# Optimization experiments

Measured on AMD Instinct MI355X. Metric: run time of the kernel, lower is better.

Reference implementation:

```python
import jax, jax.numpy as jnp
import numpy as np

N = 100000
E = 1600000
F_IN = 4
HID = 8
HEADS = 8
NEG_SLOPE = 0.2


def setup_inputs() -> dict:
    key = jax.random.key(0)
    ks = jax.random.split(key, 12)
    x = jax.random.normal(ks[0], (N, F_IN), dtype=jnp.float32)
    edge_index = jax.random.randint(ks[1], (2, E), 0, N, dtype=jnp.int64)
    s = 0.3
    W1 = jax.random.normal(ks[2], (F_IN, HEADS * HID), dtype=jnp.float32) * s
    att_src1 = jax.random.normal(ks[3], (HEADS, HID), dtype=jnp.float32) * s
    att_dst1 = jax.random.normal(ks[4], (HEADS, HID), dtype=jnp.float32) * s
    b1 = jnp.zeros((HEADS * HID,), dtype=jnp.float32)
    W2 = jax.random.normal(ks[5], (HEADS * HID, 1), dtype=jnp.float32) * s
    att_src2 = jax.random.normal(ks[6], (1, 1), dtype=jnp.float32) * s
    att_dst2 = jax.random.normal(ks[7], (1, 1), dtype=jnp.float32) * s
    b2 = jnp.zeros((1,), dtype=jnp.float32)
    return {"x": x, "edge_index": edge_index, "W1": W1, "att_src1": att_src1,
            "att_dst1": att_dst1, "b1": b1, "W2": W2, "att_src2": att_src2,
            "att_dst2": att_dst2, "b2": b2}


def gat_conv(x, src, dst, W, att_s, att_d, b, heads, out_ch, concat):
    n = x.shape[0]
    h = (x @ W).reshape(n, heads, out_ch)              # [N,H,C]
    a_s = jnp.sum(h * att_s, axis=-1)                  # [N,H]
    a_d = jnp.sum(h * att_d, axis=-1)                  # [N,H]
    e = jax.nn.leaky_relu(a_s[src] + a_d[dst], NEG_SLOPE)  # [E,H]
    # segment softmax over edges grouped by destination node
    m = jax.ops.segment_max(e, dst, num_segments=n)
    e = jnp.exp(e - m[dst])
    denom = jax.ops.segment_sum(e, dst, num_segments=n)
    alpha = e / (denom[dst] + 1e-16)                   # [E,H]
    msg = h[src] * alpha[..., None]                    # [E,H,C]
    out = jax.ops.segment_sum(msg, dst, num_segments=n)  # [N,H,C]
    out = out.reshape(n, heads * out_ch) if concat else out.mean(axis=1)
    return out + b


def reference(x, edge_index, W1, att_src1, att_dst1, b1, W2, att_src2, att_dst2, b2):
    n = x.shape[0]
    loops = jnp.arange(n, dtype=edge_index.dtype)
    src = jnp.concatenate([edge_index[0], loops])
    dst = jnp.concatenate([edge_index[1], loops])
    h = gat_conv(x, src, dst, W1, att_src1, att_dst1, b1, HEADS, HID, True)
    h = jax.nn.elu(h)
    out = gat_conv(h, src, dst, W2, att_src2, att_dst2, b2, 1, 1, False)
    return jax.nn.sigmoid(out)
```

## Files before the change

### kernel.cpp

```cpp
#include <hip/hip_runtime.h>

#define NN 100000
#define NE 1600000
#define NBKT 391
#define CAP 8192
#define TILE 4096
#define NTILE ((NE + TILE - 1) / TILE)
#define NEG 0.2f

__global__ __launch_bounds__(512) void kU_prep(
    const float* __restrict__ W1, const float* __restrict__ atts,
    const float* __restrict__ attd, float* __restrict__ us, float* __restrict__ ud,
    int* __restrict__ bcnt, int* __restrict__ row)
{
    int t = threadIdx.x;
    if (t < NBKT) bcnt[t] = 0;
    if (t == 0) row[NN] = NE;
    if (t < 64) {
        int half = t >> 5;
        int i = t & 31;
        int h = i >> 2, k = i & 3;
        const float* att = half ? attd : atts;
        float acc = 0.f;
        #pragma unroll
        for (int j = 0; j < 8; j++)
            acc += W1[k * 64 + h * 8 + j] * att[h * 8 + j];
        (half ? ud : us)[h * 4 + k] = acc;
    }
}

__global__ __launch_bounds__(1024) void kP1_tile(
    const int* __restrict__ ei, int* __restrict__ bcnt, unsigned* __restrict__ bpack)
{
    __shared__ unsigned sarr[TILE];
    __shared__ int lh[512], lsc[512], lgb[512];
    int t = threadIdx.x;
    int e0 = blockIdx.x * TILE;
    int n = NE - e0; if (n > TILE) n = TILE;

    if (t < 512) lh[t] = 0;
    __syncthreads();
    for (int i = t; i < n; i += 1024) {
        int d = ei[NE + e0 + i];
        atomicAdd(&lh[d >> 8], 1);
    }
    __syncthreads();
    if (t < 512) lsc[t] = lh[t];
    __syncthreads();
    #pragma unroll
    for (int o = 1; o < 512; o <<= 1) {
        int u = 0;
        if (t < 512 && t >= o) u = lsc[t - o];
        __syncthreads();
        if (t < 512) lsc[t] += u;
        __syncthreads();
    }
    if (t < NBKT && lh[t] > 0) lgb[t] = atomicAdd(&bcnt[t], lh[t]);
    __syncthreads();
    if (t < 512) lh[t] = lsc[t] - lh[t];
    __syncthreads();
    for (int i = t; i < n; i += 1024) {
        int s = ei[e0 + i], d = ei[NE + e0 + i];
        int b = d >> 8;
        int pos = atomicAdd(&lh[b], 1);
        sarr[pos] = ((unsigned)s << 8) | (unsigned)(d & 255);
    }
    __syncthreads();
    int wave = t >> 6, lane = t & 63;
    for (int b = wave; b < NBKT; b += 16) {
        int start = (b == 0) ? 0 : lsc[b - 1];
        int cntb = lsc[b] - start;
        if (cntb == 0) continue;
        int gb = lgb[b];
        unsigned* dstp = &bpack[(size_t)b * CAP];
        for (int j = lane; j < cntb; j += 64) {
            int gpos = gb + j;
            if (gpos < CAP) dstp[gpos] = sarr[start + j];
        }
    }
}

__global__ __launch_bounds__(1024) void kP2_build(
    const int* __restrict__ bcnt, const unsigned* __restrict__ bpack,
    int* __restrict__ row, int* __restrict__ esrc)
{
    __shared__ int lh[256], lsc[256], lcur[256];
    __shared__ int sbs[512];
    __shared__ int sarr[CAP];
    int b = blockIdx.x;
    int t = threadIdx.x;
    if (t < 512) sbs[t] = (t < b) ? bcnt[t] : 0;
    __syncthreads();
    #pragma unroll
    for (int o = 256; o > 0; o >>= 1) {
        if (t < o) sbs[t] += sbs[t + o];
        __syncthreads();
    }
    int base = sbs[0];
    int cnt = bcnt[b];
    if (cnt > CAP) cnt = CAP;
    const unsigned* bp = &bpack[(size_t)b * CAP];
    if (t < 256) lh[t] = 0;
    __syncthreads();
    for (int i = t; i < cnt; i += 1024)
        atomicAdd(&lh[bp[i] & 255u], 1);
    __syncthreads();
    if (t < 256) lsc[t] = lh[t];
    __syncthreads();
    #pragma unroll
    for (int o = 1; o < 256; o <<= 1) {
        int u = 0;
        if (t < 256 && t >= o) u = lsc[t - o];
        __syncthreads();
        if (t < 256) lsc[t] += u;
        __syncthreads();
    }
    if (t < 256) {
        int ex = lsc[t] - lh[t];
        lcur[t] = ex;
        int node = b * 256 + t;
        if (node < NN) row[node] = base + ex;
    }
    __syncthreads();
    for (int i = t; i < cnt; i += 1024) {
        unsigned u = bp[i];
        int pos = atomicAdd(&lcur[u & 255u], 1);
        sarr[pos] = (int)(u >> 8);
    }
    __syncthreads();
    for (int i = t; i < cnt; i += 1024)
        esrc[base + i] = sarr[i];
}

__global__ __launch_bounds__(256) void kE_l1agg(
    const int* __restrict__ row, const int* __restrict__ esrc,
    const float* __restrict__ x, const float* __restrict__ us,
    const float* __restrict__ ud, const float* __restrict__ W1,
    const float* __restrict__ b1, const float* __restrict__ W2,
    float* __restrict__ h2)
{
    int t = threadIdx.x;
    int grp = t >> 3;
    int h   = t & 7;
    int dst = blockIdx.x * 32 + grp;
    if (dst >= NN) return;

    int start = row[dst], end = row[dst + 1];
    int m = end - start;

    float4 u  = *reinterpret_cast<const float4*>(&us[h * 4]);
    float4 vd = *reinterpret_cast<const float4*>(&ud[h * 4]);
    float4 xd = *reinterpret_cast<const float4*>(&x[(size_t)dst * 4]);
    float adj = xd.x * vd.x + xd.y * vd.y + xd.z * vd.z + xd.w * vd.w;

    float a0 = fmaf(xd.x, u.x, fmaf(xd.y, u.y, fmaf(xd.z, u.z, fmaf(xd.w, u.w, adj))));
    a0 = fmaxf(a0, NEG * a0);
    float p0 = __expf(a0);
    float den = p0;
    float xa0 = p0 * xd.x, xa1 = p0 * xd.y, xa2 = p0 * xd.z, xa3 = p0 * xd.w;

    int j = 0;
    for (; j + 4 <= m; j += 4) {
        int s0 = esrc[start + j];
        int s1 = esrc[start + j + 1];
        int s2 = esrc[start + j + 2];
        int s3 = esrc[start + j + 3];
        float4 q0 = *reinterpret_cast<const float4*>(&x[(size_t)s0 * 4]);
        float4 q1 = *reinterpret_cast<const float4*>(&x[(size_t)s1 * 4]);
        float4 q2 = *reinterpret_cast<const float4*>(&x[(size_t)s2 * 4]);
        float4 q3 = *reinterpret_cast<const float4*>(&x[(size_t)s3 * 4]);
        float b0 = fmaf(q0.x, u.x, fmaf(q0.y, u.y, fmaf(q0.z, u.z, fmaf(q0.w, u.w, adj))));
        float b1v = fmaf(q1.x, u.x, fmaf(q1.y, u.y, fmaf(q1.z, u.z, fmaf(q1.w, u.w, adj))));
        float b2v = fmaf(q2.x, u.x, fmaf(q2.y, u.y, fmaf(q2.z, u.z, fmaf(q2.w, u.w, adj))));
        float b3v = fmaf(q3.x, u.x, fmaf(q3.y, u.y, fmaf(q3.z, u.z, fmaf(q3.w, u.w, adj))));
        b0  = fmaxf(b0,  NEG * b0);
        b1v = fmaxf(b1v, NEG * b1v);
        b2v = fmaxf(b2v, NEG * b2v);
        b3v = fmaxf(b3v, NEG * b3v);
        float pa = __expf(b0);
        float pb = __expf(b1v);
        float pc = __expf(b2v);
        float pd = __expf(b3v);
        den += (pa + pb) + (pc + pd);
        xa0 = fmaf(pa, q0.x, fmaf(pb, q1.x, fmaf(pc, q2.x, fmaf(pd, q3.x, xa0))));
        xa1 = fmaf(pa, q0.y, fmaf(pb, q1.y, fmaf(pc, q2.y, fmaf(pd, q3.y, xa1))));
        xa2 = fmaf(pa, q0.z, fmaf(pb, q1.z, fmaf(pc, q2.z, fmaf(pd, q3.z, xa2))));
        xa3 = fmaf(pa, q0.w, fmaf(pb, q1.w, fmaf(pc, q2.w, fmaf(pd, q3.w, xa3))));
    }
    for (; j < m; ++j) {
        int s0 = esrc[start + j];
        float4 q0 = *reinterpret_cast<const float4*>(&x[(size_t)s0 * 4]);
        float b0 = fmaf(q0.x, u.x, fmaf(q0.y, u.y, fmaf(q0.z, u.z, fmaf(q0.w, u.w, adj))));
        b0 = fmaxf(b0, NEG * b0);
        float pb = __expf(b0);
        den += pb;
        xa0 = fmaf(pb, q0.x, xa0);
        xa1 = fmaf(pb, q0.y, xa1);
        xa2 = fmaf(pb, q0.z, xa2);
        xa3 = fmaf(pb, q0.w, xa3);
    }

    int c0 = h * 8;
    float4 w0l = *reinterpret_cast<const float4*>(&W1[c0]);
    float4 w0h = *reinterpret_cast<const float4*>(&W1[c0 + 4]);
    float4 w1l = *reinterpret_cast<const float4*>(&W1[64 + c0]);
    float4 w1h = *reinterpret_cast<const float4*>(&W1[64 + c0 + 4]);
    float4 w2l = *reinterpret_cast<const float4*>(&W1[128 + c0]);
    float4 w2h = *reinterpret_cast<const float4*>(&W1[128 + c0 + 4]);
    float4 w3l = *reinterpret_cast<const float4*>(&W1[192 + c0]);
    float4 w3h = *reinterpret_cast<const float4*>(&W1[192 + c0 + 4]);
    float4 bbl = *reinterpret_cast<const float4*>(&b1[c0]);
    float4 bbh = *reinterpret_cast<const float4*>(&b1[c0 + 4]);
    float4 wwl = *reinterpret_cast<const float4*>(&W2[c0]);
    float4 wwh = *reinterpret_cast<const float4*>(&W2[c0 + 4]);
    float inv = 1.f / (den + 1e-16f);

    float acc = 0.f;
    {
        float v;
        v = (xa0*w0l.x + xa1*w1l.x + xa2*w2l.x + xa3*w3l.x)*inv + bbl.x;
        v = v > 0.f ? v : (__expf(v) - 1.f);  acc += v * wwl.x;
        v = (xa0*w0l.y + xa1*w1l.y + xa2*w2l.y + xa3*w3l.y)*inv + bbl.y;
        v = v > 0.f ? v : (__expf(v) - 1.f);  acc += v * wwl.y;
        v = (xa0*w0l.z + xa1*w1l.z + xa2*w2l.z + xa3*w3l.z)*inv + bbl.z;
        v = v > 0.f ? v : (__expf(v) - 1.f);  acc += v * wwl.z;
        v = (xa0*w0l.w + xa1*w1l.w + xa2*w2l.w + xa3*w3l.w)*inv + bbl.w;
        v = v > 0.f ? v : (__expf(v) - 1.f);  acc += v * wwl.w;
        v = (xa0*w0h.x + xa1*w1h.x + xa2*w2h.x + xa3*w3h.x)*inv + bbh.x;
        v = v > 0.f ? v : (__expf(v) - 1.f);  acc += v * wwh.x;
        v = (xa0*w0h.y + xa1*w1h.y + xa2*w2h.y + xa3*w3h.y)*inv + bbh.y;
        v = v > 0.f ? v : (__expf(v) - 1.f);  acc += v * wwh.y;
        v = (xa0*w0h.z + xa1*w1h.z + xa2*w2h.z + xa3*w3h.z)*inv + bbh.z;
        v = v > 0.f ? v : (__expf(v) - 1.f);  acc += v * wwh.z;
        v = (xa0*w0h.w + xa1*w1h.w + xa2*w2h.w + xa3*w3h.w)*inv + bbh.w;
        v = v > 0.f ? v : (__expf(v) - 1.f);  acc += v * wwh.w;
    }
    acc += __shfl_xor(acc, 1, 8);
    acc += __shfl_xor(acc, 2, 8);
    acc += __shfl_xor(acc, 4, 8);
    if (h == 0) h2[dst] = acc;
}

__global__ __launch_bounds__(256) void kF_l2agg(
    const int* __restrict__ row, const int* __restrict__ esrc,
    const float* __restrict__ h2, const float* __restrict__ as2,
    const float* __restrict__ ad2, const float* __restrict__ b2,
    float* __restrict__ out)
{
    int t = threadIdx.x;
    int grp = t >> 3;
    int sub = t & 7;
    int dst = blockIdx.x * 32 + grp;
    if (dst >= NN) return;
    int start = row[dst], end = row[dst + 1];
    float a_s = as2[0], a_d = ad2[0];
    float hdv = h2[dst];
    float hd = hdv * a_d;

    float den = 0.f, num = 0.f;
    if (sub == 0) {
        float v = hdv * a_s + hd;
        v = fmaxf(v, NEG * v);
        float p = __expf(v);
        den = p;
        num = p * hdv;
    }
    int i = start + sub;
    for (; i + 24 < end; i += 32) {
        float hs0 = h2[esrc[i]];
        float hs1 = h2[esrc[i + 8]];
        float hs2 = h2[esrc[i + 16]];
        float hs3 = h2[esrc[i + 24]];
        float v0 = fmaf(hs0, a_s, hd);
        float v1 = fmaf(hs1, a_s, hd);
        float v2 = fmaf(hs2, a_s, hd);
        float v3 = fmaf(hs3, a_s, hd);
        v0 = fmaxf(v0, NEG * v0);
        v1 = fmaxf(v1, NEG * v1);
        v2 = fmaxf(v2, NEG * v2);
        v3 = fmaxf(v3, NEG * v3);
        float p0 = __expf(v0);
        float p1 = __expf(v1);
        float p2 = __expf(v2);
        float p3 = __expf(v3);
        den += (p0 + p1) + (p2 + p3);
        num = fmaf(p0, hs0, fmaf(p1, hs1, fmaf(p2, hs2, fmaf(p3, hs3, num))));
    }
    for (; i < end; i += 8) {
        float hs = h2[esrc[i]];
        float v = fmaf(hs, a_s, hd);
        v = fmaxf(v, NEG * v);
        float p = __expf(v);
        den += p;
        num = fmaf(p, hs, num);
    }
    den += __shfl_xor(den, 1, 8);
    num += __shfl_xor(num, 1, 8);
    den += __shfl_xor(den, 2, 8);
    num += __shfl_xor(num, 2, 8);
    den += __shfl_xor(den, 4, 8);
    num += __shfl_xor(num, 4, 8);
    if (sub == 0) {
        float v = num / (den + 1e-16f) + b2[0];
        out[dst] = 1.f / (1.f + __expf(-v));
    }
}

extern "C" void kernel_launch(void* const* d_in, const int* in_sizes, int n_in,
                              void* d_out, int out_size, void* d_ws, size_t ws_size,
                              hipStream_t stream) {
    const float* x     = (const float*)d_in[0];
    const int*   ei    = (const int*)d_in[1];
    const float* W1    = (const float*)d_in[2];
    const float* atts1 = (const float*)d_in[3];
    const float* attd1 = (const float*)d_in[4];
    const float* b1    = (const float*)d_in[5];
    const float* W2    = (const float*)d_in[6];
    const float* atts2 = (const float*)d_in[7];
    const float* attd2 = (const float*)d_in[8];
    const float* b2    = (const float*)d_in[9];
    float* out = (float*)d_out;

    float* w = (float*)d_ws;
    float* us = w;
    float* ud = w + 32;
    float* h2 = w + 64;
    int* ibase  = (int*)(w + 64 + (size_t)NN);
    int* bcnt   = ibase;
    int* row    = ibase + 512;
    int* esrc   = ibase + 512 + NN + 64;
    unsigned* bpack = (unsigned*)(ibase + 512 + NN + 64 + NE);

    dim3 gG((NN + 31) / 32);

    hipLaunchKernelGGL(kU_prep, dim3(1), dim3(512), 0, stream, W1, atts1, attd1, us, ud, bcnt, row);
    hipLaunchKernelGGL(kP1_tile, dim3(NTILE), dim3(1024), 0, stream, ei, bcnt, bpack);
    hipLaunchKernelGGL(kP2_build, dim3(NBKT), dim3(1024), 0, stream, bcnt, bpack, row, esrc);
    hipLaunchKernelGGL(kE_l1agg, gG, dim3(256), 0, stream, row, esrc, x, us, ud, W1, b1, W2, h2);
    hipLaunchKernelGGL(kF_l2agg, gG, dim3(256), 0, stream, row, esrc, h2, atts2, attd2, b2, out);
}
```

Before: 71.66 us.

## Use fixed-capacity bucket CSR with (start,count) rows and drop prep kernel

Switches the CSR layout so each 256-node bucket gets a fixed CAP-sized slot in esrc, with each node storing (start, degree) as int2. This removes the cross-bucket prefix reduction and the shared staging buffer in the build kernel, which now scatters directly to global memory. The attention-projection prep is folded into the layer-1 kernel via shared memory, the counter reset becomes a memset, and the partition kernels drop from 1024 to 512 threads. The costs are that every layer-1 block recomputes the small projection, esrc writes become uncoalesced scatters, and edge lists become sparse in memory.

```diff
diff --git a/kernel.cpp b/kernel.cpp
--- a/kernel.cpp
+++ b/kernel.cpp
@@ -8,28 +8,7 @@
 #define NTILE ((NE + TILE - 1) / TILE)
 #define NEG 0.2f
 
-__global__ __launch_bounds__(512) void kU_prep(
-    const float* __restrict__ W1, const float* __restrict__ atts,
-    const float* __restrict__ attd, float* __restrict__ us, float* __restrict__ ud,
-    int* __restrict__ bcnt, int* __restrict__ row)
-{
-    int t = threadIdx.x;
-    if (t < NBKT) bcnt[t] = 0;
-    if (t == 0) row[NN] = NE;
-    if (t < 64) {
-        int half = t >> 5;
-        int i = t & 31;
-        int h = i >> 2, k = i & 3;
-        const float* att = half ? attd : atts;
-        float acc = 0.f;
-        #pragma unroll
-        for (int j = 0; j < 8; j++)
-            acc += W1[k * 64 + h * 8 + j] * att[h * 8 + j];
-        (half ? ud : us)[h * 4 + k] = acc;
-    }
-}
-
-__global__ __launch_bounds__(1024) void kP1_tile(
+__global__ __launch_bounds__(512) void kP1_tile(
     const int* __restrict__ ei, int* __restrict__ bcnt, unsigned* __restrict__ bpack)
 {
     __shared__ unsigned sarr[TILE];
@@ -38,28 +17,27 @@
     int e0 = blockIdx.x * TILE;
     int n = NE - e0; if (n > TILE) n = TILE;
 
-    if (t < 512) lh[t] = 0;
-    __syncthreads();
-    for (int i = t; i < n; i += 1024) {
+    lh[t] = 0;
+    __syncthreads();
+    for (int i = t; i < n; i += 512) {
         int d = ei[NE + e0 + i];
         atomicAdd(&lh[d >> 8], 1);
     }
     __syncthreads();
-    if (t < 512) lsc[t] = lh[t];
+    lsc[t] = lh[t];
     __syncthreads();
     #pragma unroll
     for (int o = 1; o < 512; o <<= 1) {
-        int u = 0;
-        if (t < 512 && t >= o) u = lsc[t - o];
+        int u = (t >= o) ? lsc[t - o] : 0;
         __syncthreads();
-        if (t < 512) lsc[t] += u;
+        lsc[t] += u;
         __syncthreads();
     }
     if (t < NBKT && lh[t] > 0) lgb[t] = atomicAdd(&bcnt[t], lh[t]);
     __syncthreads();
-    if (t < 512) lh[t] = lsc[t] - lh[t];
-    __syncthreads();
-    for (int i = t; i < n; i += 1024) {
+    lh[t] = lsc[t] - lh[t];
+    __syncthreads();
+    for (int i = t; i < n; i += 512) {
         int s = ei[e0 + i], d = ei[NE + e0 + i];
         int b = d >> 8;
         int pos = atomicAdd(&lh[b], 1);
@@ -67,7 +45,7 @@
     }
     __syncthreads();
     int wave = t >> 6, lane = t & 63;
-    for (int b = wave; b < NBKT; b += 16) {
+    for (int b = wave; b < NBKT; b += 8) {
         int start = (b == 0) ? 0 : lsc[b - 1];
         int cntb = lsc[b] - start;
         if (cntb == 0) continue;
@@ -80,29 +58,20 @@
     }
 }
 
-__global__ __launch_bounds__(1024) void kP2_build(
+__global__ __launch_bounds__(512) void kP2_build(
     const int* __restrict__ bcnt, const unsigned* __restrict__ bpack,
-    int* __restrict__ row, int* __restrict__ esrc)
+    int2* __restrict__ rowsd, int* __restrict__ esrc)
 {
     __shared__ int lh[256], lsc[256], lcur[256];
-    __shared__ int sbs[512];
-    __shared__ int sarr[CAP];
     int b = blockIdx.x;
     int t = threadIdx.x;
-    if (t < 512) sbs[t] = (t < b) ? bcnt[t] : 0;
-    __syncthreads();
-    #pragma unroll
-    for (int o = 256; o > 0; o >>= 1) {
-        if (t < o) sbs[t] += sbs[t + o];
-        __syncthreads();
-    }
-    int base = sbs[0];
     int cnt = bcnt[b];
     if (cnt > CAP) cnt = CAP;
     const unsigned* bp = &bpack[(size_t)b * CAP];
+    int base = b * CAP;
     if (t < 256) lh[t] = 0;
     __syncthreads();
-    for (int i = t; i < cnt; i += 1024)
+    for (int i = t; i < cnt; i += 512)
         atomicAdd(&lh[bp[i] & 255u], 1);
     __syncthreads();
     if (t < 256) lsc[t] = lh[t];
@@ -119,37 +88,47 @@
         int ex = lsc[t] - lh[t];
         lcur[t] = ex;
         int node = b * 256 + t;
-        if (node < NN) row[node] = base + ex;
-    }
-    __syncthreads();
-    for (int i = t; i < cnt; i += 1024) {
+        if (node < NN) rowsd[node] = make_int2(base + ex, lh[t]);
+    }
+    __syncthreads();
+    for (int i = t; i < cnt; i += 512) {
         unsigned u = bp[i];
         int pos = atomicAdd(&lcur[u & 255u], 1);
-        sarr[pos] = (int)(u >> 8);
-    }
-    __syncthreads();
-    for (int i = t; i < cnt; i += 1024)
-        esrc[base + i] = sarr[i];
+        esrc[base + pos] = (int)(u >> 8);
+    }
 }
 
 __global__ __launch_bounds__(256) void kE_l1agg(
-    const int* __restrict__ row, const int* __restrict__ esrc,
-    const float* __restrict__ x, const float* __restrict__ us,
-    const float* __restrict__ ud, const float* __restrict__ W1,
+    const int2* __restrict__ rowsd, const int* __restrict__ esrc,
+    const float* __restrict__ x, const float* __restrict__ atts,
+    const float* __restrict__ attd, const float* __restrict__ W1,
     const float* __restrict__ b1, const float* __restrict__ W2,
     float* __restrict__ h2)
 {
+    __shared__ float sus[32], sud[32];
     int t = threadIdx.x;
+    if (t < 64) {
+        int half = t >> 5;
+        int i = t & 31;
+        int hh = i >> 2, k = i & 3;
+        const float* att = half ? attd : atts;
+        float acc = 0.f;
+        #pragma unroll
+        for (int j = 0; j < 8; j++)
+            acc += W1[k * 64 + hh * 8 + j] * att[hh * 8 + j];
+        (half ? sud : sus)[hh * 4 + k] = acc;
+    }
+    __syncthreads();
+
     int grp = t >> 3;
     int h   = t & 7;
     int dst = blockIdx.x * 32 + grp;
-    if (dst >= NN) return;
-
-    int start = row[dst], end = row[dst + 1];
-    int m = end - start;
-
-    float4 u  = *reinterpret_cast<const float4*>(&us[h * 4]);
-    float4 vd = *reinterpret_cast<const float4*>(&ud[h * 4]);
+
+    int2 rd = rowsd[dst];
+    int start = rd.x, m = rd.y;
+
+    float4 u  = *reinterpret_cast<const float4*>(&sus[h * 4]);
+    float4 vd = *reinterpret_cast<const float4*>(&sud[h * 4]);
     float4 xd = *reinterpret_cast<const float4*>(&x[(size_t)dst * 4]);
     float adj = xd.x * vd.x + xd.y * vd.y + xd.z * vd.z + xd.w * vd.w;
 
@@ -242,7 +221,7 @@
 }
 
 __global__ __launch_bounds__(256) void kF_l2agg(
-    const int* __restrict__ row, const int* __restrict__ esrc,
+    const int2* __restrict__ rowsd, const int* __restrict__ esrc,
     const float* __restrict__ h2, const float* __restrict__ as2,
     const float* __restrict__ ad2, const float* __restrict__ b2,
     float* __restrict__ out)
@@ -251,8 +230,8 @@
     int grp = t >> 3;
     int sub = t & 7;
     int dst = blockIdx.x * 32 + grp;
-    if (dst >= NN) return;
-    int start = row[dst], end = row[dst + 1];
+    int2 rd = rowsd[dst];
+    int start = rd.x, end = rd.x + rd.y;
     float a_s = as2[0], a_d = ad2[0];
     float hdv = h2[dst];
     float hd = hdv * a_d;
@@ -322,20 +301,18 @@
     float* out = (float*)d_out;
 
     float* w = (float*)d_ws;
-    float* us = w;
-    float* ud = w + 32;
-    float* h2 = w + 64;
-    int* ibase  = (int*)(w + 64 + (size_t)NN);
-    int* bcnt   = ibase;
-    int* row    = ibase + 512;
-    int* esrc   = ibase + 512 + NN + 64;
-    unsigned* bpack = (unsigned*)(ibase + 512 + NN + 64 + NE);
-
-    dim3 gG((NN + 31) / 32);
-
-    hipLaunchKernelGGL(kU_prep, dim3(1), dim3(512), 0, stream, W1, atts1, attd1, us, ud, bcnt, row);
-    hipLaunchKernelGGL(kP1_tile, dim3(NTILE), dim3(1024), 0, stream, ei, bcnt, bpack);
-    hipLaunchKernelGGL(kP2_build, dim3(NBKT), dim3(1024), 0, stream, bcnt, bpack, row, esrc);
-    hipLaunchKernelGGL(kE_l1agg, gG, dim3(256), 0, stream, row, esrc, x, us, ud, W1, b1, W2, h2);
-    hipLaunchKernelGGL(kF_l2agg, gG, dim3(256), 0, stream, row, esrc, h2, atts2, attd2, b2, out);
-}
+    float* h2 = w;
+    int*  ibase = (int*)(w + (size_t)NN);
+    int2* rowsd = (int2*)ibase;
+    int*  bcnt  = ibase + (size_t)2 * NN;
+    int*  esrc  = ibase + (size_t)2 * NN + 512;
+    unsigned* bpack = (unsigned*)(esrc + (size_t)NBKT * CAP);
+
+    dim3 gG(NN / 32);
+
+    hipMemsetAsync(bcnt, 0, NBKT * sizeof(int), stream);
+    hipLaunchKernelGGL(kP1_tile, dim3(NTILE), dim3(512), 0, stream, ei, bcnt, bpack);
+    hipLaunchKernelGGL(kP2_build, dim3(NBKT), dim3(512), 0, stream, bcnt, bpack, rowsd, esrc);
+    hipLaunchKernelGGL(kE_l1agg, gG, dim3(256), 0, stream, rowsd, esrc, x, atts1, attd1, W1, b1, W2, h2);
+    hipLaunchKernelGGL(kF_l2agg, gG, dim3(256), 0, stream, rowsd, esrc, h2, atts2, attd2, b2, out);
+}
```

New measurement: 83.45 us. 16.4% more time.
